# Kernel tuning notes

Hardware: AMD Instinct MI355X
Metric: run time of the kernel (lower is better)

The kernel has to match this reference:

```python
import jax, jax.numpy as jnp
import numpy as np

B, N, D = 4, 4096, 1024
H, DH = 16, 64
EPS = 1e-5


def setup_inputs() -> dict:
    key = jax.random.key(0)
    ks = jax.random.split(key, 4)
    x = jax.random.normal(ks[0], (B, N, D), dtype=jnp.float32)
    w_qkv = jax.random.normal(ks[1], (D, 3 * H * DH), dtype=jnp.float32) * 0.02
    # per-head LayerNorm affine params (one LayerNorm(dim_head) per head)
    gamma_k = jnp.ones((H, DH), dtype=jnp.float32)
    beta_k = jnp.zeros((H, DH), dtype=jnp.float32)
    gamma_v = jnp.ones((H, DH), dtype=jnp.float32)
    beta_v = jnp.zeros((H, DH), dtype=jnp.float32)
    w_out = jax.random.normal(ks[2], (H * DH, D), dtype=jnp.float32) * 0.02
    b_out = jnp.zeros((D,), dtype=jnp.float32)
    return {"x": x, "w_qkv": w_qkv, "gamma_k": gamma_k, "beta_k": beta_k,
            "gamma_v": gamma_v, "beta_v": beta_v, "w_out": w_out, "b_out": b_out}


def _per_head_layernorm(t, gamma, beta):
    # t: [b, h, n, d]; gamma/beta: [h, d] (distinct affine per head)
    mu = jnp.mean(t, axis=-1, keepdims=True)
    var = jnp.mean(jnp.square(t - mu), axis=-1, keepdims=True)  # biased, as torch LayerNorm
    tn = (t - mu) * jax.lax.rsqrt(var + EPS)
    return tn * gamma[None, :, None, :] + beta[None, :, None, :]


def reference(x, w_qkv, gamma_k, beta_k, gamma_v, beta_v, w_out, b_out):
    b, n, _ = x.shape
    h, dh = gamma_k.shape
    qkv = jnp.einsum('bnd,de->bne', x, w_qkv)  # [b, n, 3*h*dh]
    q, k, v = jnp.split(qkv, 3, axis=-1)

    def to_heads(t):  # b n (h d) -> b h n d
        return t.reshape(b, n, h, dh).transpose(0, 2, 1, 3)

    q, k, v = to_heads(q), to_heads(k), to_heads(v)
    k = _per_head_layernorm(k, gamma_k, beta_k)
    v = _per_head_layernorm(v, gamma_v, beta_v)
    # linear attention: scores = k^T v / n  -> [b, h, d, d]
    scores = jnp.einsum('bhnd,bhne->bhde', k, v) / n
    out = jnp.einsum('bhnd,bhde->bhne', q, scores)  # [b, h, n, d]
    out = out.transpose(0, 2, 1, 3).reshape(b, n, h * dh)
    return jnp.einsum('bne,ed->bnd', out, w_out) + b_out
```

## Files before the change

### kernel.cpp

```cpp
#include <hip/hip_runtime.h>

typedef __attribute__((ext_vector_type(4))) float f32x4;
typedef __attribute__((ext_vector_type(8))) short s16x8;

#define DEV static __device__ __forceinline__

typedef __attribute__((address_space(3))) void lds_t;
typedef __attribute__((address_space(1))) void gbl_t;

DEV void gload_lds16(const void* g, void* l) {
    __builtin_amdgcn_global_load_lds((gbl_t*)g, (lds_t*)l, 16, 0, 0);
}

DEV ushort f2bf(float f) {
    unsigned u = __float_as_uint(f);
    u += 0x7fffu + ((u >> 16) & 1u);
    return (ushort)(u >> 16);
}
DEV float bf2f(ushort h) { return __uint_as_float(((unsigned)h) << 16); }

#define FULLBAR() do {                              \
    __builtin_amdgcn_sched_barrier(0);              \
    asm volatile("" ::: "memory");                  \
    __builtin_amdgcn_s_barrier();                   \
    asm volatile("" ::: "memory");                  \
    __builtin_amdgcn_sched_barrier(0);              \
} while (0)

#define WAITVM(n) asm volatile("s_waitcnt vmcnt(" #n ")" ::: "memory")

__global__ void pack_x_k(const float* __restrict__ x, ushort* __restrict__ xb, int n4) {
    int stride = gridDim.x * blockDim.x;
    for (int i = blockIdx.x * blockDim.x + threadIdx.x; i < n4; i += stride) {
        float4 v = reinterpret_cast<const float4*>(x)[i];
        ushort4 o;
        o.x = f2bf(v.x); o.y = f2bf(v.y); o.z = f2bf(v.z); o.w = f2bf(v.w);
        reinterpret_cast<ushort4*>(xb)[i] = o;
    }
}

__global__ void pack_wq_k(const float* __restrict__ w, ushort* __restrict__ o) {
    int i = blockIdx.x * 256 + threadIdx.x;
    int r = i >> 8, c4 = i & 255;
    float4 v = *reinterpret_cast<const float4*>(w + (size_t)r * 3072 + c4 * 4);
    ushort4 u;
    u.x = f2bf(v.x); u.y = f2bf(v.y); u.z = f2bf(v.z); u.w = f2bf(v.w);
    *reinterpret_cast<ushort4*>(o + (size_t)r * 1024 + c4 * 4) = u;
}

__global__ void trans_pack_k(const float* __restrict__ in, ushort* __restrict__ out,
                             int R, int C, int col0) {
    __shared__ float tile[32][33];
    int bx = col0 + blockIdx.x * 32, by = blockIdx.y * 32;
    int tx = threadIdx.x, ty = threadIdx.y;
#pragma unroll
    for (int i = 0; i < 32; i += 8)
        tile[ty + i][tx] = in[(size_t)(by + ty + i) * C + bx + tx];
    __syncthreads();
#pragma unroll
    for (int i = 0; i < 32; i += 8)
        out[(size_t)(bx - col0 + ty + i) * R + by + tx] = f2bf(tile[tx][ty + i]);
}

template <int MODE>
__global__ __launch_bounds__(256) void gemm_bt_k(
    const ushort* __restrict__ A, const ushort* __restrict__ Bt,
    int Nn, int col0, size_t b_stride, size_t a_bstride,
    ushort* __restrict__ qo, ushort* __restrict__ ko, ushort* __restrict__ vo,
    const float* __restrict__ gk, const float* __restrict__ bk,
    const float* __restrict__ gv, const float* __restrict__ bv,
    const float* __restrict__ bias, float* __restrict__ outf)
{
    __shared__ __align__(16) ushort SH[24576];
    const int t = threadIdx.x;
    const int w = t >> 6, lane = t & 63;
    const int wm = w >> 1, wn = w & 1;
    const int lrow = lane & 15, kh = lane >> 4;

    int n0, m0;
    if (MODE == 2) {
        n0 = blockIdx.x * 128; m0 = blockIdx.y * 128;
    } else {
        int bid = blockIdx.y * gridDim.x + blockIdx.x;
        int C8 = (gridDim.x * gridDim.y) >> 3;
        int nid = (bid & 7) * C8 + (bid >> 3);
        n0 = (nid % gridDim.x) * 128;
        m0 = (nid / gridDim.x) * 128;
    }

    const ushort* Ae  = (MODE == 2) ? A + blockIdx.z * a_bstride : A;
    const ushort* Bte = (MODE == 1) ? Bt + (size_t)(m0 >> 12) * b_stride : Bt;

    const int srow0 = w * 32 + (lane >> 2);
    const int scolSwz = (((lane & 3) ^ ((lane >> 3) & 3)) * 8);

    f32x4 acc[4][4] = {};

    auto STAGE = [&](int kt, int s) {
        ushort* As = SH + s * 8192;
        ushort* Bs = As + 4096;
        const ushort* Ag = Ae  + (size_t)(m0 + srow0) * 1024 + kt * 32 + scolSwz;
        const ushort* Bg = Bte + (size_t)(n0 + srow0) * 1024 + kt * 32 + scolSwz;
        gload_lds16(Ag,             As + w * 1024);
        gload_lds16(Bg,             Bs + w * 1024);
        gload_lds16(Ag + 16 * 1024, As + w * 1024 + 512);
        gload_lds16(Bg + 16 * 1024, Bs + w * 1024 + 512);
    };

    const int gsw = (lrow >> 1) & 3;
    const int rdoff = (kh ^ gsw) * 8;

    auto COMPUTE = [&](int s) {
        const ushort* As = SH + s * 8192;
        const ushort* Bs = As + 4096;
        s16x8 af[4], bfr[4];
#pragma unroll
        for (int mi = 0; mi < 4; mi++)
            af[mi] = *reinterpret_cast<const s16x8*>(&As[(wm * 64 + mi * 16 + lrow) * 32 + rdoff]);
#pragma unroll
        for (int ni = 0; ni < 4; ni++)
            bfr[ni] = *reinterpret_cast<const s16x8*>(&Bs[(wn * 64 + ni * 16 + lrow) * 32 + rdoff]);
#pragma unroll
        for (int mi = 0; mi < 4; mi++)
#pragma unroll
            for (int ni = 0; ni < 4; ni++)
                acc[mi][ni] = __builtin_amdgcn_mfma_f32_16x16x32_bf16(af[mi], bfr[ni], acc[mi][ni], 0, 0, 0);
    };

    STAGE(0, 0);
    STAGE(1, 1);
    int ss = 2, sc_ = 0;
    for (int kt = 0; kt < 30; ++kt) {
        STAGE(kt + 2, ss);
        ss = (ss == 2) ? 0 : ss + 1;
        WAITVM(8);
        FULLBAR();
        COMPUTE(sc_);
        sc_ = (sc_ == 2) ? 0 : sc_ + 1;
        FULLBAR();
    }
    WAITVM(4); FULLBAR(); COMPUTE(0); FULLBAR();
    WAITVM(0); FULLBAR(); COMPUTE(1);

    if (MODE == 0) {
        const int e0 = col0 + n0 + wn * 64;
        const int which = e0 >> 10;
        const int h = (e0 >> 6) & 15;
        const float* g  = (which == 1) ? gk : gv;
        const float* bb = (which == 1) ? bk : bv;
        ushort* dst     = (which == 1) ? ko : vo;
        float gr[4], br[4];
#pragma unroll
        for (int ni = 0; ni < 4; ni++) {
            gr[ni] = g[h * 64 + ni * 16 + lrow];
            br[ni] = bb[h * 64 + ni * 16 + lrow];
        }
        __syncthreads();
        ushort* Tl = SH + w * 4608;
#pragma unroll
        for (int mi = 0; mi < 4; mi++)
#pragma unroll
            for (int j = 0; j < 4; j++) {
                float s = acc[mi][0][j] + acc[mi][1][j] + acc[mi][2][j] + acc[mi][3][j];
                s += __shfl_xor(s, 1, 64);
                s += __shfl_xor(s, 2, 64);
                s += __shfl_xor(s, 4, 64);
                s += __shfl_xor(s, 8, 64);
                float mu = s * (1.f / 64.f);
                float t2 = 0.f;
#pragma unroll
                for (int ni = 0; ni < 4; ni++) {
                    float dd = acc[mi][ni][j] - mu;
                    t2 += dd * dd;
                }
                t2 += __shfl_xor(t2, 1, 64);
                t2 += __shfl_xor(t2, 2, 64);
                t2 += __shfl_xor(t2, 4, 64);
                t2 += __shfl_xor(t2, 8, 64);
                float inv = rsqrtf(t2 * (1.f / 64.f) + 1e-5f);
#pragma unroll
                for (int ni = 0; ni < 4; ni++) {
                    float y = (acc[mi][ni][j] - mu) * inv * gr[ni] + br[ni];
                    Tl[(ni * 16 + lrow) * 72 + mi * 16 + kh * 4 + j] = f2bf(y);
                }
            }
        const int mrow0 = m0 + wm * 64;
        const int b = mrow0 >> 12, ns0 = mrow0 & 4095;
        ushort* obase = dst + (((size_t)b * 16 + h) * 64) * 4096 + ns0;
#pragma unroll
        for (int p = 0; p < 8; ++p) {
            int d = p * 8 + (lane >> 3);
            int mo = (lane & 7) * 8;
            s16x8 vv = *reinterpret_cast<const s16x8*>(&Tl[d * 72 + mo]);
            *reinterpret_cast<s16x8*>(obase + (size_t)d * 4096 + mo) = vv;
        }
    } else if (MODE == 1) {
#pragma unroll
        for (int mi = 0; mi < 4; mi++)
#pragma unroll
            for (int ni = 0; ni < 4; ni++) {
                int e = n0 + wn * 64 + ni * 16 + lrow;
                float bv2 = bias[e];
#pragma unroll
                for (int j = 0; j < 4; j++) {
                    int m = m0 + wm * 64 + mi * 16 + kh * 4 + j;
                    outf[(size_t)m * Nn + e] = acc[mi][ni][j] + bv2;
                }
            }
    } else {
        ushort* o = qo + (size_t)blockIdx.z * 1048576;
#pragma unroll
        for (int mi = 0; mi < 4; mi++)
#pragma unroll
            for (int ni = 0; ni < 4; ni++) {
                int e = n0 + wn * 64 + ni * 16 + lrow;
#pragma unroll
                for (int j = 0; j < 4; j++) {
                    int m = m0 + wm * 64 + mi * 16 + kh * 4 + j;
                    o[(size_t)m * 1024 + e] = f2bf(acc[mi][ni][j]);
                }
            }
    }
}

__global__ __launch_bounds__(256) void scores_k(const ushort* __restrict__ kT,
                                                const ushort* __restrict__ vT,
                                                float* __restrict__ sc)
{
    __shared__ float red[4][64][65];
    const int bh = blockIdx.y;
    const int t = threadIdx.x;
    const int w = t >> 6, lane = t & 63;
    const int lrow = lane & 15, kh = lane >> 4;
    const ushort* ka = kT + (size_t)bh * 64 * 4096;
    const ushort* va = vT + (size_t)bh * 64 * 4096;
    const int n0 = blockIdx.x * 512 + w * 128;

    f32x4 acc[4][4] = {};
#pragma unroll
    for (int ks = 0; ks < 4; ++ks) {
        const int n = n0 + ks * 32 + kh * 8;
        s16x8 af[4], bfr[4];
#pragma unroll
        for (int mi = 0; mi < 4; mi++)
            af[mi] = *reinterpret_cast<const s16x8*>(ka + (size_t)(mi * 16 + lrow) * 4096 + n);
#pragma unroll
        for (int ni = 0; ni < 4; ni++)
            bfr[ni] = *reinterpret_cast<const s16x8*>(va + (size_t)(ni * 16 + lrow) * 4096 + n);
#pragma unroll
        for (int mi = 0; mi < 4; mi++)
#pragma unroll
            for (int ni = 0; ni < 4; ni++)
                acc[mi][ni] = __builtin_amdgcn_mfma_f32_16x16x32_bf16(af[mi], bfr[ni], acc[mi][ni], 0, 0, 0);
    }
#pragma unroll
    for (int mi = 0; mi < 4; mi++)
#pragma unroll
        for (int ni = 0; ni < 4; ni++)
#pragma unroll
            for (int j = 0; j < 4; j++)
                red[w][mi * 16 + kh * 4 + j][ni * 16 + lrow] = acc[mi][ni][j];
    __syncthreads();
    const float scale = 1.f / 4096.f;
    for (int idx = t; idx < 4096; idx += 256) {
        int d = idx >> 6, e = idx & 63;
        float s = red[0][d][e] + red[1][d][e] + red[2][d][e] + red[3][d][e];
        atomicAdd(&sc[(size_t)bh * 4096 + idx], s * scale);
    }
}

__global__ __launch_bounds__(256) void wprime_k(const float* __restrict__ sc,
                                                const ushort* __restrict__ woutT,
                                                ushort* __restrict__ wpT)
{
    __shared__ float scl[64][65];
    __shared__ ushort wl[128][72];
    int bh = blockIdx.y;
    int b = bh >> 4, h = bh & 15;
    int f0 = blockIdx.x * 128;
    int t = threadIdx.x;
    for (int i = t; i < 4096; i += 256) {
        int d2 = i >> 6, e = i & 63;
        scl[e][d2] = sc[(size_t)bh * 4096 + i];
    }
    for (int i = t; i < 1024; i += 256) {
        int fl = i >> 3, c = i & 7;
        *reinterpret_cast<int4*>(&wl[fl][c * 8]) =
            *reinterpret_cast<const int4*>(woutT + (size_t)(f0 + fl) * 1024 + h * 64 + c * 8);
    }
    __syncthreads();
    int dd = (t & 7) * 8;
    int fl0 = t >> 3;
#pragma unroll
    for (int fi = 0; fi < 4; ++fi) {
        int fl = fi * 32 + fl0;
        float acc[8] = {};
        for (int e = 0; e < 64; ++e) {
            float wv = bf2f(wl[fl][e]);
#pragma unroll
            for (int i = 0; i < 8; ++i)
                acc[i] = fmaf(wv, scl[e][dd + i], acc[i]);
        }
        ushort4 o0, o1;
        o0.x = f2bf(acc[0]); o0.y = f2bf(acc[1]); o0.z = f2bf(acc[2]); o0.w = f2bf(acc[3]);
        o1.x = f2bf(acc[4]); o1.y = f2bf(acc[5]); o1.z = f2bf(acc[6]); o1.w = f2bf(acc[7]);
        ushort* op = wpT + ((size_t)b * 1024 + f0 + fl) * 1024 + h * 64 + dd;
        *reinterpret_cast<ushort4*>(op) = o0;
        *reinterpret_cast<ushort4*>(op + 4) = o1;
    }
}

extern "C" void kernel_launch(void* const* d_in, const int* in_sizes, int n_in,
                              void* d_out, int out_size, void* d_ws, size_t ws_size,
                              hipStream_t stream)
{
    const float* x       = (const float*)d_in[0];
    const float* w_qkv   = (const float*)d_in[1];
    const float* gamma_k = (const float*)d_in[2];
    const float* beta_k  = (const float*)d_in[3];
    const float* gamma_v = (const float*)d_in[4];
    const float* beta_v  = (const float*)d_in[5];
    const float* w_out   = (const float*)d_in[6];
    const float* b_out   = (const float*)d_in[7];
    float* out = (float*)d_out;

    char* ws = (char*)d_ws;
    const size_t MB = 1024 * 1024;
    ushort* xb    = (ushort*)(ws);
    ushort* wkvT  = (ushort*)(ws + 32 * MB);
    ushort* woutT = (ushort*)(ws + 38 * MB);
    ushort* wqb   = (ushort*)(ws + 40 * MB);
    ushort* kb    = (ushort*)(ws + 48 * MB);
    ushort* vb    = (ushort*)(ws + 80 * MB);
    float*  sc    = (float*)(ws + 112 * MB);
    ushort* wpT   = (ushort*)(ws + 120 * MB);
    ushort* fT    = (ushort*)(ws + 128 * MB);

    pack_x_k<<<2048, 256, 0, stream>>>(x, xb, 16384 * 1024 / 4);
    pack_wq_k<<<1024, 256, 0, stream>>>(w_qkv, wqb);
    trans_pack_k<<<dim3(64, 32), dim3(32, 8), 0, stream>>>(w_qkv, wkvT, 1024, 3072, 1024);
    trans_pack_k<<<dim3(32, 32), dim3(32, 8), 0, stream>>>(w_out, woutT, 1024, 1024, 0);
    gemm_bt_k<0><<<dim3(16, 128), 256, 0, stream>>>(xb, wkvT, 2048, 1024, 0, 0,
                                                    nullptr, kb, vb,
                                                    gamma_k, beta_k, gamma_v, beta_v,
                                                    nullptr, nullptr);
    hipMemsetAsync(sc, 0, 64 * 4096 * sizeof(float), stream);
    scores_k<<<dim3(8, 64), 256, 0, stream>>>(kb, vb, sc);
    wprime_k<<<dim3(8, 64), 256, 0, stream>>>(sc, woutT, wpT);
    gemm_bt_k<2><<<dim3(8, 8, 4), 256, 0, stream>>>(wpT, wqb, 1024, 0, 0, (size_t)1048576,
                                                    fT, nullptr, nullptr,
                                                    nullptr, nullptr, nullptr, nullptr,
                                                    nullptr, nullptr);
    gemm_bt_k<1><<<dim3(8, 128), 256, 0, stream>>>(xb, fT, 1024, 0, (size_t)1048576, 0,
                                                   nullptr, nullptr, nullptr,
                                                   nullptr, nullptr, nullptr, nullptr,
                                                   b_out, out);
}
```

Measured before the change: 227.8 us.

## Widen GEMM block tile to 128x256 with two-head LayerNorm epilogue

Each GEMM block now covers 256 output columns instead of 128, so each wave holds a 64x128 accumulator. Every A fragment now feeds twice as many MFMAs, and grids halve. The staging loop loads 6 16-byte chunks per thread per stage, and the LDS ring grows to 3x24KB. The K/V epilogue now computes LayerNorm for two heads per wave and writes both transposed tiles. This doubles accumulator registers (launch bounds ask for 2 blocks/SM), raising spill or occupancy risk, and fewer blocks may underfill the GPU for the smaller GEMMs.

```diff
diff --git a/kernel.cpp b/kernel.cpp
--- a/kernel.cpp
+++ b/kernel.cpp
@@ -63,7 +63,7 @@
 }
 
 template <int MODE>
-__global__ __launch_bounds__(256) void gemm_bt_k(
+__global__ __launch_bounds__(256, 2) void gemm_bt_k(
     const ushort* __restrict__ A, const ushort* __restrict__ Bt,
     int Nn, int col0, size_t b_stride, size_t a_bstride,
     ushort* __restrict__ qo, ushort* __restrict__ ko, ushort* __restrict__ vo,
@@ -71,7 +71,7 @@
     const float* __restrict__ gv, const float* __restrict__ bv,
     const float* __restrict__ bias, float* __restrict__ outf)
 {
-    __shared__ __align__(16) ushort SH[24576];
+    __shared__ __align__(16) ushort SH[36864];
     const int t = threadIdx.x;
     const int w = t >> 6, lane = t & 63;
     const int wm = w >> 1, wn = w & 1;
@@ -79,51 +79,52 @@
 
     int n0, m0;
     if (MODE == 2) {
-        n0 = blockIdx.x * 128; m0 = blockIdx.y * 128;
+        n0 = blockIdx.x * 256; m0 = blockIdx.y * 128;
     } else {
         int bid = blockIdx.y * gridDim.x + blockIdx.x;
         int C8 = (gridDim.x * gridDim.y) >> 3;
         int nid = (bid & 7) * C8 + (bid >> 3);
-        n0 = (nid % gridDim.x) * 128;
+        n0 = (nid % gridDim.x) * 256;
         m0 = (nid / gridDim.x) * 128;
     }
 
     const ushort* Ae  = (MODE == 2) ? A + blockIdx.z * a_bstride : A;
     const ushort* Bte = (MODE == 1) ? Bt + (size_t)(m0 >> 12) * b_stride : Bt;
 
-    const int srow0 = w * 32 + (lane >> 2);
+    const int srow = lane >> 2;
     const int scolSwz = (((lane & 3) ^ ((lane >> 3) & 3)) * 8);
 
-    f32x4 acc[4][4] = {};
+    f32x4 acc[4][8] = {};
 
     auto STAGE = [&](int kt, int s) {
-        ushort* As = SH + s * 8192;
+        ushort* As = SH + s * 12288;
         ushort* Bs = As + 4096;
-        const ushort* Ag = Ae  + (size_t)(m0 + srow0) * 1024 + kt * 32 + scolSwz;
-        const ushort* Bg = Bte + (size_t)(n0 + srow0) * 1024 + kt * 32 + scolSwz;
-        gload_lds16(Ag,             As + w * 1024);
-        gload_lds16(Bg,             Bs + w * 1024);
-        gload_lds16(Ag + 16 * 1024, As + w * 1024 + 512);
-        gload_lds16(Bg + 16 * 1024, Bs + w * 1024 + 512);
+        const ushort* Ag = Ae  + (size_t)(m0 + w * 16 + srow) * 1024 + kt * 32 + scolSwz;
+        const ushort* Bg = Bte + (size_t)(n0 + w * 16 + srow) * 1024 + kt * 32 + scolSwz;
+        gload_lds16(Ag,              As + w * 512);
+        gload_lds16(Ag + 64 * 1024,  As + w * 512 + 2048);
+        gload_lds16(Bg,              Bs + w * 512);
+        gload_lds16(Bg + 64 * 1024,  Bs + w * 512 + 2048);
+        gload_lds16(Bg + 128 * 1024, Bs + w * 512 + 4096);
+        gload_lds16(Bg + 192 * 1024, Bs + w * 512 + 6144);
     };
 
-    const int gsw = (lrow >> 1) & 3;
-    const int rdoff = (kh ^ gsw) * 8;
+    const int rdoff = (kh ^ ((lrow >> 1) & 3)) * 8;
 
     auto COMPUTE = [&](int s) {
-        const ushort* As = SH + s * 8192;
+        const ushort* As = SH + s * 12288;
         const ushort* Bs = As + 4096;
-        s16x8 af[4], bfr[4];
+        s16x8 af[4], bfr[8];
 #pragma unroll
         for (int mi = 0; mi < 4; mi++)
             af[mi] = *reinterpret_cast<const s16x8*>(&As[(wm * 64 + mi * 16 + lrow) * 32 + rdoff]);
 #pragma unroll
-        for (int ni = 0; ni < 4; ni++)
-            bfr[ni] = *reinterpret_cast<const s16x8*>(&Bs[(wn * 64 + ni * 16 + lrow) * 32 + rdoff]);
-#pragma unroll
-        for (int mi = 0; mi < 4; mi++)
-#pragma unroll
-            for (int ni = 0; ni < 4; ni++)
+        for (int ni = 0; ni < 8; ni++)
+            bfr[ni] = *reinterpret_cast<const s16x8*>(&Bs[(wn * 128 + ni * 16 + lrow) * 32 + rdoff]);
+#pragma unroll
+        for (int mi = 0; mi < 4; mi++)
+#pragma unroll
+            for (int ni = 0; ni < 8; ni++)
                 acc[mi][ni] = __builtin_amdgcn_mfma_f32_16x16x32_bf16(af[mi], bfr[ni], acc[mi][ni], 0, 0, 0);
     };
 
@@ -133,73 +134,96 @@
     for (int kt = 0; kt < 30; ++kt) {
         STAGE(kt + 2, ss);
         ss = (ss == 2) ? 0 : ss + 1;
-        WAITVM(8);
+        WAITVM(12);
         FULLBAR();
         COMPUTE(sc_);
         sc_ = (sc_ == 2) ? 0 : sc_ + 1;
         FULLBAR();
     }
-    WAITVM(4); FULLBAR(); COMPUTE(0); FULLBAR();
+    WAITVM(6); FULLBAR(); COMPUTE(0); FULLBAR();
     WAITVM(0); FULLBAR(); COMPUTE(1);
 
     if (MODE == 0) {
-        const int e0 = col0 + n0 + wn * 64;
+        const int e0 = col0 + n0 + wn * 128;
         const int which = e0 >> 10;
-        const int h = (e0 >> 6) & 15;
+        const int h0 = (e0 >> 6) & 15;
         const float* g  = (which == 1) ? gk : gv;
         const float* bb = (which == 1) ? bk : bv;
         ushort* dst     = (which == 1) ? ko : vo;
-        float gr[4], br[4];
-#pragma unroll
-        for (int ni = 0; ni < 4; ni++) {
-            gr[ni] = g[h * 64 + ni * 16 + lrow];
-            br[ni] = bb[h * 64 + ni * 16 + lrow];
+        float gr[8], br[8];
+#pragma unroll
+        for (int ni = 0; ni < 8; ni++) {
+            int gi = (h0 + (ni >> 2)) * 64 + (ni & 3) * 16 + lrow;
+            gr[ni] = g[gi];
+            br[ni] = bb[gi];
         }
         __syncthreads();
-        ushort* Tl = SH + w * 4608;
+        ushort* Tl = SH + w * 9216;
 #pragma unroll
         for (int mi = 0; mi < 4; mi++)
 #pragma unroll
             for (int j = 0; j < 4; j++) {
-                float s = acc[mi][0][j] + acc[mi][1][j] + acc[mi][2][j] + acc[mi][3][j];
-                s += __shfl_xor(s, 1, 64);
-                s += __shfl_xor(s, 2, 64);
-                s += __shfl_xor(s, 4, 64);
-                s += __shfl_xor(s, 8, 64);
-                float mu = s * (1.f / 64.f);
-                float t2 = 0.f;
+                float s0 = acc[mi][0][j] + acc[mi][1][j] + acc[mi][2][j] + acc[mi][3][j];
+                s0 += __shfl_xor(s0, 1, 64);
+                s0 += __shfl_xor(s0, 2, 64);
+                s0 += __shfl_xor(s0, 4, 64);
+                s0 += __shfl_xor(s0, 8, 64);
+                float mu0 = s0 * (1.f / 64.f);
+                float t0 = 0.f;
 #pragma unroll
                 for (int ni = 0; ni < 4; ni++) {
-                    float dd = acc[mi][ni][j] - mu;
-                    t2 += dd * dd;
-                }
-                t2 += __shfl_xor(t2, 1, 64);
-                t2 += __shfl_xor(t2, 2, 64);
-                t2 += __shfl_xor(t2, 4, 64);
-                t2 += __shfl_xor(t2, 8, 64);
-                float inv = rsqrtf(t2 * (1.f / 64.f) + 1e-5f);
-#pragma unroll
-                for (int ni = 0; ni < 4; ni++) {
+                    float dd = acc[mi][ni][j] - mu0;
+                    t0 += dd * dd;
+                }
+                t0 += __shfl_xor(t0, 1, 64);
+                t0 += __shfl_xor(t0, 2, 64);
+                t0 += __shfl_xor(t0, 4, 64);
+                t0 += __shfl_xor(t0, 8, 64);
+                float inv0 = rsqrtf(t0 * (1.f / 64.f) + 1e-5f);
+                float s1 = acc[mi][4][j] + acc[mi][5][j] + acc[mi][6][j] + acc[mi][7][j];
+                s1 += __shfl_xor(s1, 1, 64);
+                s1 += __shfl_xor(s1, 2, 64);
+                s1 += __shfl_xor(s1, 4, 64);
+                s1 += __shfl_xor(s1, 8, 64);
+                float mu1 = s1 * (1.f / 64.f);
+                float t1 = 0.f;
+#pragma unroll
+                for (int ni = 4; ni < 8; ni++) {
+                    float dd = acc[mi][ni][j] - mu1;
+                    t1 += dd * dd;
+                }
+                t1 += __shfl_xor(t1, 1, 64);
+                t1 += __shfl_xor(t1, 2, 64);
+                t1 += __shfl_xor(t1, 4, 64);
+                t1 += __shfl_xor(t1, 8, 64);
+                float inv1 = rsqrtf(t1 * (1.f / 64.f) + 1e-5f);
+#pragma unroll
+                for (int ni = 0; ni < 8; ni++) {
+                    float mu = (ni < 4) ? mu0 : mu1;
+                    float inv = (ni < 4) ? inv0 : inv1;
                     float y = (acc[mi][ni][j] - mu) * inv * gr[ni] + br[ni];
                     Tl[(ni * 16 + lrow) * 72 + mi * 16 + kh * 4 + j] = f2bf(y);
                 }
             }
         const int mrow0 = m0 + wm * 64;
         const int b = mrow0 >> 12, ns0 = mrow0 & 4095;
-        ushort* obase = dst + (((size_t)b * 16 + h) * 64) * 4096 + ns0;
-#pragma unroll
-        for (int p = 0; p < 8; ++p) {
-            int d = p * 8 + (lane >> 3);
-            int mo = (lane & 7) * 8;
-            s16x8 vv = *reinterpret_cast<const s16x8*>(&Tl[d * 72 + mo]);
-            *reinterpret_cast<s16x8*>(obase + (size_t)d * 4096 + mo) = vv;
+#pragma unroll
+        for (int hh = 0; hh < 2; ++hh) {
+            ushort* obase = dst + (((size_t)b * 16 + h0 + hh) * 64) * 4096 + ns0;
+#pragma unroll
+            for (int p = 0; p < 8; ++p) {
+                int d = p * 8 + (lane >> 3);
+                int mo = (lane & 7) * 8;
+                s16x8 vv = *reinterpret_cast<const s16x8*>(&Tl[(hh * 64 + d) * 72 + mo]);
+                *reinterpret_cast<s16x8*>(obase + (size_t)d * 4096 + mo) = vv;
+            }
         }
     } else if (MODE == 1) {
 #pragma unroll
         for (int mi = 0; mi < 4; mi++)
 #pragma unroll
-            for (int ni = 0; ni < 4; ni++) {
-                int e = n0 + wn * 64 + ni * 16 + lrow;
+            for (int ni = 0; ni < 8; ni++) {
+                int e = n0 + wn * 128 + ni * 16 + lrow;
                 float bv2 = bias[e];
 #pragma unroll
                 for (int j = 0; j < 4; j++) {
@@ -212,8 +236,8 @@
 #pragma unroll
         for (int mi = 0; mi < 4; mi++)
 #pragma unroll
-            for (int ni = 0; ni < 4; ni++) {
-                int e = n0 + wn * 64 + ni * 16 + lrow;
+            for (int ni = 0; ni < 8; ni++) {
+                int e = n0 + wn * 128 + ni * 16 + lrow;
 #pragma unroll
                 for (int j = 0; j < 4; j++) {
                     int m = m0 + wm * 64 + mi * 16 + kh * 4 + j;
@@ -340,18 +364,18 @@
     pack_wq_k<<<1024, 256, 0, stream>>>(w_qkv, wqb);
     trans_pack_k<<<dim3(64, 32), dim3(32, 8), 0, stream>>>(w_qkv, wkvT, 1024, 3072, 1024);
     trans_pack_k<<<dim3(32, 32), dim3(32, 8), 0, stream>>>(w_out, woutT, 1024, 1024, 0);
-    gemm_bt_k<0><<<dim3(16, 128), 256, 0, stream>>>(xb, wkvT, 2048, 1024, 0, 0,
-                                                    nullptr, kb, vb,
-                                                    gamma_k, beta_k, gamma_v, beta_v,
-                                                    nullptr, nullptr);
+    gemm_bt_k<0><<<dim3(8, 128), 256, 0, stream>>>(xb, wkvT, 2048, 1024, 0, 0,
+                                                   nullptr, kb, vb,
+                                                   gamma_k, beta_k, gamma_v, beta_v,
+                                                   nullptr, nullptr);
     hipMemsetAsync(sc, 0, 64 * 4096 * sizeof(float), stream);
     scores_k<<<dim3(8, 64), 256, 0, stream>>>(kb, vb, sc);
     wprime_k<<<dim3(8, 64), 256, 0, stream>>>(sc, woutT, wpT);
-    gemm_bt_k<2><<<dim3(8, 8, 4), 256, 0, stream>>>(wpT, wqb, 1024, 0, 0, (size_t)1048576,
+    gemm_bt_k<2><<<dim3(4, 8, 4), 256, 0, stream>>>(wpT, wqb, 1024, 0, 0, (size_t)1048576,
                                                     fT, nullptr, nullptr,
                                                     nullptr, nullptr, nullptr, nullptr,
                                                     nullptr, nullptr);
-    gemm_bt_k<1><<<dim3(8, 128), 256, 0, stream>>>(xb, fT, 1024, 0, (size_t)1048576, 0,
+    gemm_bt_k<1><<<dim3(4, 128), 256, 0, stream>>>(xb, fT, 1024, 0, (size_t)1048576, 0,
                                                    nullptr, nullptr, nullptr,
                                                    nullptr, nullptr, nullptr, nullptr,
                                                    b_out, out);
```

Measured after the change: 224.4 us. No clear change (-1.5%).
